# Kernel optimization log

Hardware: AMD Instinct MI355X
Metric: run time of the kernel (lower is better)

The kernel has to match this reference:

```python
import jax, jax.numpy as jnp
import numpy as np

N_EXPERTS = 64
TOP_K = 2
DIM = 2048
N_TOKENS = 32768
SCALE = 1.0


def setup_inputs() -> dict:
    key = jax.random.key(0)
    k1, k2 = jax.random.split(key)
    x = jax.random.normal(k1, (N_TOKENS, DIM), dtype=jnp.float32)
    gate_w = jax.random.normal(k2, (N_EXPERTS, DIM), dtype=jnp.float32) * (1.0 / np.sqrt(DIM))
    return {"x": x, "gate_w": gate_w}


def reference(x, gate_w):
    # logits: (N, E) = x @ W^T, scaled
    logits = jnp.einsum("nd,ed->ne", x, gate_w) * SCALE
    topk_weights, expert_indices = jax.lax.top_k(logits, TOP_K)  # (N, k)
    topk_weights = jax.nn.softmax(topk_weights, axis=-1)
    # scatter ones at selected experts -> binary mask (N, E)
    expert_mask = jax.nn.one_hot(expert_indices, N_EXPERTS, dtype=logits.dtype).sum(axis=-2)
    return expert_mask, topk_weights, expert_indices
```

## Files before the change

kernel.cpp:

```cpp
#include <hip/hip_runtime.h>
#include <float.h>

#define NT 32768
#define DIM 2048
#define NE 64
#define TAU 1e-3f
#define TPB 32
#define CHUNK 64
#define NCH (DIM / CHUNK)

typedef __attribute__((ext_vector_type(8))) short short8;
typedef __attribute__((ext_vector_type(4))) float f32x4;

__device__ __forceinline__ unsigned short f2bf(float f) {
    unsigned u = __float_as_uint(f);
    u += 0x7fffu + ((u >> 16) & 1u);
    return (unsigned short)(u >> 16);
}
__device__ __forceinline__ float bf2f(unsigned short h) {
    return __uint_as_float(((unsigned)h) << 16);
}

__global__ __launch_bounds__(256)
void prep_w(const float* __restrict__ gw, unsigned short* __restrict__ wph,
            unsigned short* __restrict__ wpl, int* __restrict__ cnt) {
    const int gid  = blockIdx.x * 256 + threadIdx.x;
    const int lane = gid & 63;
    const int ksg  = (gid >> 6) & 63;
    const int et   = gid >> 12;
    const int e    = et * 16 + (lane & 15);
    const int k0   = ksg * 32 + (lane >> 4) * 8;

    float4 v0 = *(const float4*)(gw + (size_t)e * DIM + k0);
    float4 v1 = *(const float4*)(gw + (size_t)e * DIM + k0 + 4);
    float xf[8] = {v0.x, v0.y, v0.z, v0.w, v1.x, v1.y, v1.z, v1.w};
    short8 h, l;
#pragma unroll
    for (int j = 0; j < 8; ++j) {
        unsigned short hh = f2bf(xf[j]);
        h[j] = (short)hh;
        l[j] = (short)f2bf(xf[j] - bf2f(hh));
    }
    *(short8*)(wph + (size_t)gid * 8) = h;
    *(short8*)(wpl + (size_t)gid * 8) = l;
    if (gid == 0) *cnt = 0;
}

__global__ __launch_bounds__(256, 4)
void router_mfma(const float* __restrict__ x,
                 const unsigned short* __restrict__ wph,
                 const unsigned short* __restrict__ wpl,
                 float* __restrict__ out,
                 int* __restrict__ cnt, int* __restrict__ list) {
    __shared__ __align__(16) unsigned char smem[16384];

    const int tid  = threadIdx.x;
    const int lane = tid & 63;
    const int wid  = tid >> 6;
    const int tg   = wid >> 1;
    const int eg   = wid & 1;
    const int t0   = blockIdx.x * TPB;

    const int r  = tid >> 3;
    const int sq = tid & 7;
    const int g  = r >> 4;
    const int sr = r & 15;
    const unsigned swoff = (unsigned)((sr * 128 + sq * 16) ^ ((sr & 7) << 4));
    const float* xbase = x + (size_t)(t0 + r) * DIM + sq * 8;
    unsigned char* stb = smem + g * 2048 + swoff;

    const unsigned roff0 = (unsigned)((((lane & 15) * 128) | ((lane >> 4) << 4))
                                      ^ ((lane & 7) << 4));
    const unsigned roff1 = roff0 ^ 64u;

    f32x4 accP[2], accQ[2];
#pragma unroll
    for (int e = 0; e < 2; ++e)
#pragma unroll
        for (int j = 0; j < 4; ++j) { accP[e][j] = 0.f; accQ[e][j] = 0.f; }

    float4 xr0, xr1;
    short8 Bh[2][2], Bl[2][2];

#define LOADX(c_) { xr0 = *(const float4*)(xbase + (c_) * CHUNK); \
                    xr1 = *(const float4*)(xbase + (c_) * CHUNK + 4); }

#define BLOAD(c_) { _Pragma("unroll") for (int e = 0; e < 2; ++e) \
    _Pragma("unroll") for (int ks = 0; ks < 2; ++ks) { \
        size_t o_ = (((size_t)(eg * 2 + e) * 64 + ((c_) * 2 + ks)) * 64 + lane) * 8; \
        Bh[e][ks] = *(const short8*)(wph + o_); \
        Bl[e][ks] = *(const short8*)(wpl + o_); } }

#define CVT_STORE(buf_) { \
        unsigned u0 = __float_as_uint(xr0.x), u1 = __float_as_uint(xr0.y); \
        unsigned u2 = __float_as_uint(xr0.z), u3 = __float_as_uint(xr0.w); \
        unsigned u4 = __float_as_uint(xr1.x), u5 = __float_as_uint(xr1.y); \
        unsigned u6 = __float_as_uint(xr1.z), u7 = __float_as_uint(xr1.w); \
        float l0 = xr0.x - __uint_as_float(u0 & 0xffff0000u); \
        float l1 = xr0.y - __uint_as_float(u1 & 0xffff0000u); \
        float l2 = xr0.z - __uint_as_float(u2 & 0xffff0000u); \
        float l3 = xr0.w - __uint_as_float(u3 & 0xffff0000u); \
        float l4 = xr1.x - __uint_as_float(u4 & 0xffff0000u); \
        float l5 = xr1.y - __uint_as_float(u5 & 0xffff0000u); \
        float l6 = xr1.z - __uint_as_float(u6 & 0xffff0000u); \
        float l7 = xr1.w - __uint_as_float(u7 & 0xffff0000u); \
        ushort4 h0_ = make_ushort4((unsigned short)(u0 >> 16), (unsigned short)(u1 >> 16), \
                                   (unsigned short)(u2 >> 16), (unsigned short)(u3 >> 16)); \
        ushort4 h1_ = make_ushort4((unsigned short)(u4 >> 16), (unsigned short)(u5 >> 16), \
                                   (unsigned short)(u6 >> 16), (unsigned short)(u7 >> 16)); \
        ushort4 lo0_ = make_ushort4((unsigned short)(__float_as_uint(l0) >> 16), \
                                    (unsigned short)(__float_as_uint(l1) >> 16), \
                                    (unsigned short)(__float_as_uint(l2) >> 16), \
                                    (unsigned short)(__float_as_uint(l3) >> 16)); \
        ushort4 lo1_ = make_ushort4((unsigned short)(__float_as_uint(l4) >> 16), \
                                    (unsigned short)(__float_as_uint(l5) >> 16), \
                                    (unsigned short)(__float_as_uint(l6) >> 16), \
                                    (unsigned short)(__float_as_uint(l7) >> 16)); \
        unsigned char* p_ = stb + (buf_) * 8192; \
        *(ushort4*)(p_)          = h0_;  *(ushort4*)(p_ + 8)        = h1_; \
        *(ushort4*)(p_ + 4096)   = lo0_; *(ushort4*)(p_ + 4096 + 8) = lo1_; }

#define MFMA_PHASE(buf_) { _Pragma("unroll") for (int ks = 0; ks < 2; ++ks) { \
        const unsigned char* pa_ = smem + (buf_) * 8192 + tg * 2048 \
                                   + (ks ? roff1 : roff0); \
        short8 Ah_ = *(const short8*)pa_; \
        short8 Al_ = *(const short8*)(pa_ + 4096); \
        _Pragma("unroll") for (int e = 0; e < 2; ++e) { \
            accP[e] = __builtin_amdgcn_mfma_f32_16x16x32_bf16(Ah_, Bh[e][ks], accP[e], 0, 0, 0); \
            accQ[e] = __builtin_amdgcn_mfma_f32_16x16x32_bf16(Ah_, Bl[e][ks], accQ[e], 0, 0, 0); \
            accQ[e] = __builtin_amdgcn_mfma_f32_16x16x32_bf16(Al_, Bh[e][ks], accQ[e], 0, 0, 0); } } }

    LOADX(0)
    CVT_STORE(0)
    __syncthreads();

#pragma unroll 1
    for (int c = 0; c < NCH; ++c) {
        if (c + 1 < NCH) LOADX(c + 1)
        BLOAD(c)
        MFMA_PHASE(c & 1)
        if (c + 1 < NCH) CVT_STORE((c + 1) & 1)
        __syncthreads();
    }
#undef LOADX
#undef BLOAD
#undef CVT_STORE
#undef MFMA_PHASE

    float* lmf = (float*)smem;
#pragma unroll
    for (int e = 0; e < 2; ++e)
#pragma unroll
        for (int jr = 0; jr < 4; ++jr)
            lmf[(tg * 16 + (lane >> 4) * 4 + jr) * 68 + eg * 32 + e * 16 + (lane & 15)] =
                accP[e][jr] + accQ[e][jr];
    __syncthreads();

    float* mout = out;
    float* wout = out + (size_t)NT * NE;
    float* iout = wout + (size_t)NT * 2;

    const int t   = tid >> 3;
    const int s   = tid & 7;
    const int tok = t0 + t;

    float vv[8];
    {
        float4 p0 = *(const float4*)&lmf[t * 68 + s * 8];
        float4 p1 = *(const float4*)&lmf[t * 68 + s * 8 + 4];
        vv[0] = p0.x; vv[1] = p0.y; vv[2] = p0.z; vv[3] = p0.w;
        vv[4] = p1.x; vv[5] = p1.y; vv[6] = p1.z; vv[7] = p1.w;
    }

    float m1 = -FLT_MAX, m2 = -FLT_MAX, m3 = -FLT_MAX;
    int   i1 = NE, i2 = NE, i3 = NE;
    auto ins = [&](float v, int e) {
        bool b1 = (v > m1) || (v == m1 && e < i1);
        bool b2 = (v > m2) || (v == m2 && e < i2);
        bool b3 = (v > m3) || (v == m3 && e < i3);
        if (b1)      { m3 = m2; i3 = i2; m2 = m1; i2 = i1; m1 = v; i1 = e; }
        else if (b2) { m3 = m2; i3 = i2; m2 = v; i2 = e; }
        else if (b3) { m3 = v; i3 = e; }
    };
#pragma unroll
    for (int j = 0; j < 8; ++j) ins(vv[j], s * 8 + j);
#pragma unroll
    for (int off = 1; off <= 4; off <<= 1) {
        float om1 = __shfl_xor(m1, off, 64); int oi1 = __shfl_xor(i1, off, 64);
        float om2 = __shfl_xor(m2, off, 64); int oi2 = __shfl_xor(i2, off, 64);
        float om3 = __shfl_xor(m3, off, 64); int oi3 = __shfl_xor(i3, off, 64);
        ins(om1, oi1); ins(om2, oi2); ins(om3, oi3);
    }

    float ed  = expf(m2 - m1);
    float inv = 1.f / (1.f + ed);

    {
        float4 mv0, mv1;
        int e0 = s * 8;
        mv0.x = (e0     == i1 || e0     == i2) ? 1.f : 0.f;
        mv0.y = (e0 + 1 == i1 || e0 + 1 == i2) ? 1.f : 0.f;
        mv0.z = (e0 + 2 == i1 || e0 + 2 == i2) ? 1.f : 0.f;
        mv0.w = (e0 + 3 == i1 || e0 + 3 == i2) ? 1.f : 0.f;
        mv1.x = (e0 + 4 == i1 || e0 + 4 == i2) ? 1.f : 0.f;
        mv1.y = (e0 + 5 == i1 || e0 + 5 == i2) ? 1.f : 0.f;
        mv1.z = (e0 + 6 == i1 || e0 + 6 == i2) ? 1.f : 0.f;
        mv1.w = (e0 + 7 == i1 || e0 + 7 == i2) ? 1.f : 0.f;
        *(float4*)(mout + (size_t)tok * NE + e0)     = mv0;
        *(float4*)(mout + (size_t)tok * NE + e0 + 4) = mv1;
    }

    if (s == 0) {
        *(float2*)(wout + 2 * tok) = make_float2(inv, ed * inv);
        *(float2*)(iout + 2 * tok) = make_float2((float)i1, (float)i2);
        if ((m1 - m2 < TAU) || (m2 - m3 < TAU)) {
            int slot = atomicAdd(cnt, 1);
            list[slot] = tok;
        }
    }
}

__global__ __launch_bounds__(256)
void repair(const float* __restrict__ x, const float* __restrict__ gw,
            float* __restrict__ out, const int* __restrict__ cnt,
            const int* __restrict__ list) {
    __shared__ float red[64][5];
    const int n   = *cnt;
    const int tid = threadIdx.x;
    const int e   = tid & 63, qq = tid >> 6;

    float* mout = out;
    float* wout = out + (size_t)NT * NE;
    float* iout = wout + (size_t)NT * 2;

    for (int i = blockIdx.x; i < n; i += gridDim.x) {
        const int tok = list[i];
        const float* xr = x + (size_t)tok * DIM + qq * 512;
        const float* wr = gw + (size_t)e * DIM + qq * 512;
        float a = 0.f;
        for (int j = 0; j < 512; j += 4) {
            float4 xv = *(const float4*)(xr + j);
            float4 wv = *(const float4*)(wr + j);
            a = fmaf(xv.x, wv.x, a); a = fmaf(xv.y, wv.y, a);
            a = fmaf(xv.z, wv.z, a); a = fmaf(xv.w, wv.w, a);
        }
        red[e][qq] = a;
        __syncthreads();
        if (tid < 64) {
            float v = ((red[e][0] + red[e][1]) + red[e][2]) + red[e][3];
            float m1 = v, m2 = -FLT_MAX; int i1 = e, i2 = NE;
#pragma unroll
            for (int off = 1; off <= 32; off <<= 1) {
                float om1 = __shfl_xor(m1, off, 64); int oi1 = __shfl_xor(i1, off, 64);
                float om2 = __shfl_xor(m2, off, 64); int oi2 = __shfl_xor(i2, off, 64);
                bool selfFirst = (m1 > om1) || (m1 == om1 && i1 < oi1);
                if (selfFirst) {
                    if (!((m2 > om1) || (m2 == om1 && i2 < oi1))) { m2 = om1; i2 = oi1; }
                } else {
                    bool c = (m1 > om2) || (m1 == om2 && i1 < oi2);
                    if (c) { m2 = m1; i2 = i1; } else { m2 = om2; i2 = oi2; }
                    m1 = om1; i1 = oi1;
                }
            }
            float ed  = expf(m2 - m1);
            float inv = 1.f / (1.f + ed);
            mout[(size_t)tok * NE + e] = (e == i1 || e == i2) ? 1.f : 0.f;
            if (e == 0) {
                *(float2*)(wout + 2 * tok) = make_float2(inv, ed * inv);
                *(float2*)(iout + 2 * tok) = make_float2((float)i1, (float)i2);
            }
        }
        __syncthreads();
    }
}

extern "C" void kernel_launch(void* const* d_in, const int* in_sizes, int n_in,
                              void* d_out, int out_size, void* d_ws, size_t ws_size,
                              hipStream_t stream) {
    const float* x  = (const float*)d_in[0];
    const float* gw = (const float*)d_in[1];
    float* out = (float*)d_out;

    unsigned short* wph = (unsigned short*)d_ws;
    unsigned short* wpl = wph + (size_t)NE * DIM;
    int* cnt  = (int*)(wpl + (size_t)NE * DIM);
    int* list = cnt + 1;

    prep_w<<<dim3(64), dim3(256), 0, stream>>>(gw, wph, wpl, cnt);
    router_mfma<<<dim3(NT / TPB), dim3(256), 0, stream>>>(x, wph, wpl, out, cnt, list);
    repair<<<dim3(256), dim3(256), 0, stream>>>(x, gw, out, cnt, list);
}
```

Before: 109.9 us.

## Enlarge router tile to 64 tokens with fp32 LDS staging and split-on-read

Each block now handles 64 tokens with 512 threads. Each wave covers 32 tokens and one 16-expert slice, so every weight fragment loaded from global memory feeds twice as many tokens. x is staged in LDS as raw fp32 with a new swizzle, and the bf16 hi/lo split happens when MFMA operands are read rather than before the store. Weight fragments are double-buffered in registers through a manually unrolled loop, and barriers use a hand-written waitcnt/s_barrier sequence. The cost is twice the LDS footprint, more split arithmetic per read, and heavier register pressure.

```diff
diff --git a/kernel.cpp b/kernel.cpp
--- a/kernel.cpp
+++ b/kernel.cpp
@@ -5,7 +5,6 @@
 #define DIM 2048
 #define NE 64
 #define TAU 1e-3f
-#define TPB 32
 #define CHUNK 64
 #define NCH (DIM / CHUNK)
 
@@ -46,114 +45,122 @@
     if (gid == 0) *cnt = 0;
 }
 
-__global__ __launch_bounds__(256, 4)
+__device__ __forceinline__ void split8(float4 a0, float4 a1, short8& h, short8& l) {
+    float f[8] = {a0.x, a0.y, a0.z, a0.w, a1.x, a1.y, a1.z, a1.w};
+#pragma unroll
+    for (int j = 0; j < 8; ++j) {
+        unsigned u = __float_as_uint(f[j]);
+        h[j] = (short)(unsigned short)(u >> 16);
+        float lo = f[j] - __uint_as_float(u & 0xffff0000u);
+        l[j] = (short)(unsigned short)(__float_as_uint(lo) >> 16);
+    }
+}
+
+__global__ __launch_bounds__(512, 4)
 void router_mfma(const float* __restrict__ x,
                  const unsigned short* __restrict__ wph,
                  const unsigned short* __restrict__ wpl,
                  float* __restrict__ out,
                  int* __restrict__ cnt, int* __restrict__ list) {
-    __shared__ __align__(16) unsigned char smem[16384];
+    __shared__ __align__(16) unsigned char smem[32768];
 
     const int tid  = threadIdx.x;
     const int lane = tid & 63;
-    const int wid  = tid >> 6;
-    const int tg   = wid >> 1;
-    const int eg   = wid & 1;
-    const int t0   = blockIdx.x * TPB;
-
-    const int r  = tid >> 3;
-    const int sq = tid & 7;
-    const int g  = r >> 4;
-    const int sr = r & 15;
-    const unsigned swoff = (unsigned)((sr * 128 + sq * 16) ^ ((sr & 7) << 4));
-    const float* xbase = x + (size_t)(t0 + r) * DIM + sq * 8;
-    unsigned char* stb = smem + g * 2048 + swoff;
-
-    const unsigned roff0 = (unsigned)((((lane & 15) * 128) | ((lane >> 4) << 4))
-                                      ^ ((lane & 7) << 4));
-    const unsigned roff1 = roff0 ^ 64u;
+    const int wid  = __builtin_amdgcn_readfirstlane(tid >> 6);
+    const int tg   = wid >> 2;
+    const int et   = wid & 3;
+    const int t0   = blockIdx.x * 64;
+
+    const int stok = tid >> 3;
+    const int sg   = tid & 7;
+    const unsigned st_off = (unsigned)(stok * 256 + ((sg * 32) ^ ((stok & 7) << 5)));
+    const float* xrow = x + (size_t)(t0 + stok) * DIM + sg * 8;
+
+    const unsigned swz = (unsigned)((lane & 7) << 5);
+    unsigned rbase[2], koff[2];
+#pragma unroll
+    for (int tt = 0; tt < 2; ++tt)
+        rbase[tt] = (unsigned)((tg * 32 + tt * 16 + (lane & 15)) * 256);
+#pragma unroll
+    for (int kg = 0; kg < 2; ++kg)
+        koff[kg] = (unsigned)((kg * 128 + (lane >> 4) * 32)) ^ swz;
 
     f32x4 accP[2], accQ[2];
 #pragma unroll
-    for (int e = 0; e < 2; ++e)
-#pragma unroll
-        for (int j = 0; j < 4; ++j) { accP[e][j] = 0.f; accQ[e][j] = 0.f; }
-
-    float4 xr0, xr1;
-    short8 Bh[2][2], Bl[2][2];
-
-#define LOADX(c_) { xr0 = *(const float4*)(xbase + (c_) * CHUNK); \
-                    xr1 = *(const float4*)(xbase + (c_) * CHUNK + 4); }
-
-#define BLOAD(c_) { _Pragma("unroll") for (int e = 0; e < 2; ++e) \
-    _Pragma("unroll") for (int ks = 0; ks < 2; ++ks) { \
-        size_t o_ = (((size_t)(eg * 2 + e) * 64 + ((c_) * 2 + ks)) * 64 + lane) * 8; \
-        Bh[e][ks] = *(const short8*)(wph + o_); \
-        Bl[e][ks] = *(const short8*)(wpl + o_); } }
-
-#define CVT_STORE(buf_) { \
-        unsigned u0 = __float_as_uint(xr0.x), u1 = __float_as_uint(xr0.y); \
-        unsigned u2 = __float_as_uint(xr0.z), u3 = __float_as_uint(xr0.w); \
-        unsigned u4 = __float_as_uint(xr1.x), u5 = __float_as_uint(xr1.y); \
-        unsigned u6 = __float_as_uint(xr1.z), u7 = __float_as_uint(xr1.w); \
-        float l0 = xr0.x - __uint_as_float(u0 & 0xffff0000u); \
-        float l1 = xr0.y - __uint_as_float(u1 & 0xffff0000u); \
-        float l2 = xr0.z - __uint_as_float(u2 & 0xffff0000u); \
-        float l3 = xr0.w - __uint_as_float(u3 & 0xffff0000u); \
-        float l4 = xr1.x - __uint_as_float(u4 & 0xffff0000u); \
-        float l5 = xr1.y - __uint_as_float(u5 & 0xffff0000u); \
-        float l6 = xr1.z - __uint_as_float(u6 & 0xffff0000u); \
-        float l7 = xr1.w - __uint_as_float(u7 & 0xffff0000u); \
-        ushort4 h0_ = make_ushort4((unsigned short)(u0 >> 16), (unsigned short)(u1 >> 16), \
-                                   (unsigned short)(u2 >> 16), (unsigned short)(u3 >> 16)); \
-        ushort4 h1_ = make_ushort4((unsigned short)(u4 >> 16), (unsigned short)(u5 >> 16), \
-                                   (unsigned short)(u6 >> 16), (unsigned short)(u7 >> 16)); \
-        ushort4 lo0_ = make_ushort4((unsigned short)(__float_as_uint(l0) >> 16), \
-                                    (unsigned short)(__float_as_uint(l1) >> 16), \
-                                    (unsigned short)(__float_as_uint(l2) >> 16), \
-                                    (unsigned short)(__float_as_uint(l3) >> 16)); \
-        ushort4 lo1_ = make_ushort4((unsigned short)(__float_as_uint(l4) >> 16), \
-                                    (unsigned short)(__float_as_uint(l5) >> 16), \
-                                    (unsigned short)(__float_as_uint(l6) >> 16), \
-                                    (unsigned short)(__float_as_uint(l7) >> 16)); \
-        unsigned char* p_ = stb + (buf_) * 8192; \
-        *(ushort4*)(p_)          = h0_;  *(ushort4*)(p_ + 8)        = h1_; \
-        *(ushort4*)(p_ + 4096)   = lo0_; *(ushort4*)(p_ + 4096 + 8) = lo1_; }
-
-#define MFMA_PHASE(buf_) { _Pragma("unroll") for (int ks = 0; ks < 2; ++ks) { \
-        const unsigned char* pa_ = smem + (buf_) * 8192 + tg * 2048 \
-                                   + (ks ? roff1 : roff0); \
-        short8 Ah_ = *(const short8*)pa_; \
-        short8 Al_ = *(const short8*)(pa_ + 4096); \
-        _Pragma("unroll") for (int e = 0; e < 2; ++e) { \
-            accP[e] = __builtin_amdgcn_mfma_f32_16x16x32_bf16(Ah_, Bh[e][ks], accP[e], 0, 0, 0); \
-            accQ[e] = __builtin_amdgcn_mfma_f32_16x16x32_bf16(Ah_, Bl[e][ks], accQ[e], 0, 0, 0); \
-            accQ[e] = __builtin_amdgcn_mfma_f32_16x16x32_bf16(Al_, Bh[e][ks], accQ[e], 0, 0, 0); } } }
+    for (int tt = 0; tt < 2; ++tt)
+#pragma unroll
+        for (int j = 0; j < 4; ++j) { accP[tt][j] = 0.f; accQ[tt][j] = 0.f; }
+
+    float4 xa, xb;
+    short8 Bh0[2], Bl0[2], Bh1[2], Bl1[2];
+
+#define LOADX(c_) { xa = *(const float4*)(xrow + (c_) * CHUNK); \
+                    xb = *(const float4*)(xrow + (c_) * CHUNK + 4); }
+
+#define STOREX(buf_) { unsigned char* p_ = smem + (buf_) * 16384 + st_off; \
+                       *(float4*)p_ = xa; *(float4*)(p_ + 16) = xb; }
+
+#define BLOAD(bk_, c_) { _Pragma("unroll") for (int kg = 0; kg < 2; ++kg) { \
+        size_t o_ = (((size_t)et * 64 + ((c_) * 2 + kg)) * 64 + lane) * 8; \
+        Bh##bk_[kg] = *(const short8*)(wph + o_); \
+        Bl##bk_[kg] = *(const short8*)(wpl + o_); } }
+
+#define MFMA_PHASE(buf_, bk_) { _Pragma("unroll") for (int tt = 0; tt < 2; ++tt) \
+    _Pragma("unroll") for (int kg = 0; kg < 2; ++kg) { \
+        const unsigned char* pa_ = smem + (buf_) * 16384 + rbase[tt] + koff[kg]; \
+        float4 a0_ = *(const float4*)pa_; \
+        float4 a1_ = *(const float4*)(pa_ + 16); \
+        short8 Ah_, Al_; \
+        split8(a0_, a1_, Ah_, Al_); \
+        accP[tt] = __builtin_amdgcn_mfma_f32_16x16x32_bf16(Ah_, Bh##bk_[kg], accP[tt], 0, 0, 0); \
+        accQ[tt] = __builtin_amdgcn_mfma_f32_16x16x32_bf16(Ah_, Bl##bk_[kg], accQ[tt], 0, 0, 0); \
+        accQ[tt] = __builtin_amdgcn_mfma_f32_16x16x32_bf16(Al_, Bh##bk_[kg], accQ[tt], 0, 0, 0); } }
+
+#define BARSYNC { asm volatile("s_waitcnt lgkmcnt(0)" ::: "memory"); \
+                  __builtin_amdgcn_sched_barrier(0); \
+                  __builtin_amdgcn_s_barrier(); }
 
     LOADX(0)
-    CVT_STORE(0)
+    BLOAD(0, 0)
+    STOREX(0)
+    BARSYNC
+
+#pragma unroll 1
+    for (int cc = 0; cc < 15; ++cc) {
+        const int c0 = 2 * cc;
+        LOADX(c0 + 1)
+        BLOAD(1, c0 + 1)
+        MFMA_PHASE(0, 0)
+        STOREX(1)
+        BARSYNC
+        const int c1 = c0 + 1;
+        LOADX(c1 + 1)
+        BLOAD(0, c1 + 1)
+        MFMA_PHASE(1, 1)
+        STOREX(0)
+        BARSYNC
+    }
+    LOADX(31)
+    BLOAD(1, 31)
+    MFMA_PHASE(0, 0)
+    STOREX(1)
+    BARSYNC
+    MFMA_PHASE(1, 1)
     __syncthreads();
 
-#pragma unroll 1
-    for (int c = 0; c < NCH; ++c) {
-        if (c + 1 < NCH) LOADX(c + 1)
-        BLOAD(c)
-        MFMA_PHASE(c & 1)
-        if (c + 1 < NCH) CVT_STORE((c + 1) & 1)
-        __syncthreads();
-    }
 #undef LOADX
+#undef STOREX
 #undef BLOAD
-#undef CVT_STORE
 #undef MFMA_PHASE
+#undef BARSYNC
 
     float* lmf = (float*)smem;
 #pragma unroll
-    for (int e = 0; e < 2; ++e)
+    for (int tt = 0; tt < 2; ++tt)
 #pragma unroll
         for (int jr = 0; jr < 4; ++jr)
-            lmf[(tg * 16 + (lane >> 4) * 4 + jr) * 68 + eg * 32 + e * 16 + (lane & 15)] =
-                accP[e][jr] + accQ[e][jr];
+            lmf[(tg * 32 + tt * 16 + (lane >> 4) * 4 + jr) * 68 + et * 16 + (lane & 15)] =
+                accP[tt][jr] + accQ[tt][jr];
     __syncthreads();
 
     float* mout = out;
@@ -287,6 +294,6 @@
     int* list = cnt + 1;
 
     prep_w<<<dim3(64), dim3(256), 0, stream>>>(gw, wph, wpl, cnt);
-    router_mfma<<<dim3(NT / TPB), dim3(256), 0, stream>>>(x, wph, wpl, out, cnt, list);
+    router_mfma<<<dim3(NT / 64), dim3(512), 0, stream>>>(x, wph, wpl, out, cnt, list);
     repair<<<dim3(256), dim3(256), 0, stream>>>(x, gw, out, cnt, list);
 }
```

After: 98.07 us. 1.12x faster.
